# Optimization experiments

Hardware: AMD Instinct MI355X
Metric: run time of the kernel (lower is better)

The kernel has to match this reference:

```python
import jax, jax.numpy as jnp
import numpy as np

U = 100000
I = 100000
N = U + I          # total nodes
D = 64             # emb_size
E = 2000000        # nnz of normalized adjacency
B = 4096           # lookup batch
N_LAYERS = 3
ALPHA = 0.1
BETA = 0.9


def _spmm(rows, cols, vals, x):
    # y = A @ x for COO sparse A: y[r] += v * x[c]
    return jax.ops.segment_sum(vals[:, None] * x[cols], rows, num_segments=N)


def setup_inputs() -> dict:
    key = jax.random.key(0)
    ks = jax.random.split(key, 7)
    users = jax.random.randint(ks[0], (B,), 0, U, dtype=jnp.int32)
    items = jax.random.randint(ks[1], (B,), 0, I, dtype=jnp.int32)
    # xavier-uniform-ish init
    lim = float(np.sqrt(6.0 / (U + D)))
    user_emb = jax.random.uniform(ks[2], (U, D), jnp.float32, -lim, lim)
    item_emb = jax.random.uniform(ks[3], (I, D), jnp.float32, -lim, lim)
    adj_rows = jax.random.randint(ks[4], (E,), 0, N, dtype=jnp.int32)
    adj_cols = jax.random.randint(ks[5], (E,), 0, N, dtype=jnp.int32)
    # normalized adjacency values are small positives ~ 1/sqrt(deg_i*deg_j)
    adj_vals = jax.random.uniform(ks[6], (E,), jnp.float32, 0.0, 0.2)
    return {"users": users, "items": items, "user_emb": user_emb,
            "item_emb": item_emb, "adj_rows": adj_rows,
            "adj_cols": adj_cols, "adj_vals": adj_vals}


def reference(users, items, user_emb, item_emb, adj_rows, adj_cols, adj_vals):
    gamma = BETA ** N_LAYERS + ALPHA * sum(BETA ** i for i in range(N_LAYERS))
    ego = jnp.concatenate([user_emb, item_emb], axis=0)  # [N, D]
    x0 = jnp.zeros_like(ego)
    for k in range(N_LAYERS):
        ego = _spmm(adj_rows, adj_cols, adj_vals, ego)
        if k == 0:
            x0 = ego
        else:
            ego = ego * BETA + x0 * ALPHA
    ego = ego / gamma
    user_e = ego[:U][users]   # [B, D]
    item_e = ego[U:][items]   # [B, D]
    return (user_e, item_e)
```

## Files before the change

### kernel.cpp

```cpp
#include <hip/hip_runtime.h>
#include <hip/hip_fp16.h>

#define D 64
#define BETA 0.9f
#define ALPHA 0.1f
#define CB_SHIFT 10
#define CB_ROWS 1024
#define CAP_SHIFT 14
#define CAP (1 << CAP_SHIFT)

typedef __attribute__((ext_vector_type(16))) int int16v;

__global__ void concat_half(const float* __restrict__ u, const float* __restrict__ it,
                            long long UD, long long ND, __half* __restrict__ x) {
    long long n4 = ND >> 2;
    long long stride = (long long)gridDim.x * blockDim.x;
    for (long long i4 = (long long)blockIdx.x * blockDim.x + threadIdx.x; i4 < n4;
         i4 += stride) {
        long long base = i4 << 2;
        float4 v = (base < UD) ? ((const float4*)u)[i4]
                               : ((const float4*)it)[(base - UD) >> 2];
        __half2* dst = (__half2*)(x + base);
        dst[0] = __floats2half2_rn(v.x, v.y);
        dst[1] = __floats2half2_rn(v.z, v.w);
    }
}

__global__ void stageA(const int* __restrict__ rows, const int* __restrict__ cols,
                       const float* __restrict__ vals, int E,
                       int* __restrict__ gcur, int2* __restrict__ tmp) {
    __shared__ int hist[256];
    __shared__ int cur[256];
    int t = threadIdx.x;
    if (t < 256) hist[t] = 0;
    __syncthreads();
    int chunk = (E + gridDim.x - 1) / gridDim.x;
    int beg = blockIdx.x * chunk;
    int end = min(beg + chunk, E);
    for (int e = beg + t; e < end; e += blockDim.x)
        atomicAdd(&hist[rows[e] >> CB_SHIFT], 1);
    __syncthreads();
    if (t < 256) {
        int h = hist[t];
        cur[t] = h ? atomicAdd(&gcur[t], h) : 0;
    }
    __syncthreads();
    for (int e = beg + t; e < end; e += blockDim.x) {
        int r = rows[e];
        int cb = r >> CB_SHIFT;
        int p = atomicAdd(&cur[cb], 1);
        tmp[((size_t)cb << CAP_SHIFT) + p] =
            make_int2(cols[e] | ((r & (CB_ROWS - 1)) << 18), __float_as_int(vals[e]));
    }
}

__global__ void stageB(const int* __restrict__ bcnt, int N,
                       const int2* __restrict__ tmp,
                       int2* __restrict__ epack, int2* __restrict__ meta) {
    __shared__ int sc[CB_ROWS];
    __shared__ int cur[CB_ROWS];
    int cb = blockIdx.x;
    int t = threadIdx.x;
    size_t base = (size_t)cb << CAP_SHIFT;
    int nb = bcnt[cb];
    sc[t] = 0;
    __syncthreads();
    for (int e = t; e < nb; e += CB_ROWS)
        atomicAdd(&sc[((unsigned)tmp[base + e].x) >> 18], 1);
    __syncthreads();
    int mycnt = sc[t];
    for (int off = 1; off < CB_ROWS; off <<= 1) {
        int v = (t >= off) ? sc[t - off] : 0;
        __syncthreads();
        sc[t] += v;
        __syncthreads();
    }
    int excl = sc[t] - mycnt;
    cur[t] = excl;
    int r = (cb << CB_SHIFT) + t;
    if (r < N) meta[r] = make_int2((int)base + excl, mycnt);
    __syncthreads();
    for (int e = t; e < nb; e += CB_ROWS) {
        int2 pk = tmp[base + e];
        int rl = ((unsigned)pk.x) >> 18;
        int p = atomicAdd(&cur[rl], 1);
        epack[base + p] = make_int2(pk.x & ((1 << 18) - 1), pk.y);
    }
}

__device__ __forceinline__ float row_dot_s(const int2* __restrict__ ep,
                                           int beg, int cnt,
                                           const __half* __restrict__ x, int lane) {
    float acc = 0.f;
    int full = cnt & ~7;
    int e = 0;
    for (; e < full; e += 8) {
        int16v ed;
        asm volatile("s_load_dwordx16 %0, %1, 0x0\n\ts_waitcnt lgkmcnt(0)"
                     : "=s"(ed)
                     : "s"(ep + beg + e));
#define EDGEF(k)                                                              \
        acc += __int_as_float(ed[2 * (k) + 1]) *                              \
               __half2float(x[((size_t)ed[2 * (k)] << 6) + lane]);
        EDGEF(0) EDGEF(1) EDGEF(2) EDGEF(3) EDGEF(4) EDGEF(5) EDGEF(6) EDGEF(7)
#undef EDGEF
    }
    if (e < cnt) {
        int16v ed;
        asm volatile("s_load_dwordx16 %0, %1, 0x0\n\ts_waitcnt lgkmcnt(0)"
                     : "=s"(ed)
                     : "s"(ep + beg + e));
        int rem = cnt - e;
#define EDGET(k)                                                              \
        {                                                                     \
            int col = ((k) < rem) ? ed[2 * (k)] : 0;                          \
            float v = ((k) < rem) ? __int_as_float(ed[2 * (k) + 1]) : 0.0f;   \
            float xv = __half2float(x[((size_t)col << 6) + lane]);            \
            acc += ((k) < rem) ? v * xv : 0.0f;                               \
        }
        EDGET(0) EDGET(1) EDGET(2) EDGET(3) EDGET(4) EDGET(5) EDGET(6) EDGET(7)
#undef EDGET
    }
    return acc;
}

__global__ void spmm_l0(const int2* __restrict__ meta, const int2* __restrict__ epack,
                        const __half* __restrict__ xcat, int N, __half* __restrict__ y,
                        __half* __restrict__ ego1_row0) {
    int lane = threadIdx.x & 63;
    if (blockIdx.x == 0 && threadIdx.x < D)
        ego1_row0[threadIdx.x] = __float2half(0.0f);
    int r = blockIdx.x * (blockDim.x >> 6) + (threadIdx.x >> 6);
    if (r >= N) return;
    r = __builtin_amdgcn_readfirstlane(r);
    int2 m = meta[r];
    int beg = __builtin_amdgcn_readfirstlane(m.x);
    int cnt = __builtin_amdgcn_readfirstlane(m.y);
    float acc = row_dot_s(epack, beg, cnt, xcat, lane);
    y[((size_t)r << 6) + lane] = __float2half(acc);
}

__global__ void mark_flag2(const int* __restrict__ users, const int* __restrict__ items,
                           int B, int U, const int2* __restrict__ meta,
                           const int2* __restrict__ epack, int* __restrict__ flag2) {
    int lane = threadIdx.x & 63;
    int w = blockIdx.x * (blockDim.x >> 6) + (threadIdx.x >> 6);
    if (w >= 2 * B) return;
    int r = (w < B) ? users[w] : U + items[w - B];
    int2 m = meta[r];
    for (int e = m.x + lane; e < m.x + m.y; e += 64)
        flag2[epack[e].x] = 1;
}

__global__ void spmm_l1(const int2* __restrict__ meta, const int2* __restrict__ epack,
                        const __half* __restrict__ x0, const int* __restrict__ flag2,
                        int N, __half* __restrict__ y) {
    int lane = threadIdx.x & 63;
    int r = blockIdx.x * (blockDim.x >> 6) + (threadIdx.x >> 6);
    if (r >= N) return;
    r = __builtin_amdgcn_readfirstlane(r);
    if (flag2[r] == 0) return;
    int2 m = meta[r];
    int beg = __builtin_amdgcn_readfirstlane(m.x);
    int cnt = __builtin_amdgcn_readfirstlane(m.y);
    float acc = row_dot_s(epack, beg, cnt, x0, lane);
    float x0v = __half2float(x0[((size_t)r << 6) + lane]);
    y[((size_t)r << 6) + lane] = __float2half(BETA * acc + ALPHA * x0v);
}

__global__ void out_slots(const int* __restrict__ users, const int* __restrict__ items,
                          int B, int U,
                          const int2* __restrict__ meta, const int2* __restrict__ epack,
                          const __half* __restrict__ ego1, const __half* __restrict__ x0,
                          float inv_gamma, float* __restrict__ out) {
    int lane = threadIdx.x & 63;
    int w = blockIdx.x * (blockDim.x >> 6) + (threadIdx.x >> 6);
    if (w >= 2 * B) return;
    int r = (w < B) ? users[w] : U + items[w - B];
    r = __builtin_amdgcn_readfirstlane(r);
    int2 m = meta[r];
    int beg = __builtin_amdgcn_readfirstlane(m.x);
    int cnt = __builtin_amdgcn_readfirstlane(m.y);
    float acc = row_dot_s(epack, beg, cnt, ego1, lane);
    float x0v = __half2float(x0[((size_t)r << 6) + lane]);
    out[((size_t)w << 6) + lane] = (BETA * acc + ALPHA * x0v) * inv_gamma;
}

extern "C" void kernel_launch(void* const* d_in, const int* in_sizes, int n_in,
                              void* d_out, int out_size, void* d_ws, size_t ws_size,
                              hipStream_t stream) {
    const int*   users = (const int*)d_in[0];
    const int*   items = (const int*)d_in[1];
    const float* uemb  = (const float*)d_in[2];
    const float* iemb  = (const float*)d_in[3];
    const int*   arows = (const int*)d_in[4];
    const int*   acols = (const int*)d_in[5];
    const float* avals = (const float*)d_in[6];

    const int B = in_sizes[0];
    const int U = in_sizes[2] / D;
    const int I = in_sizes[3] / D;
    const int N = U + I;
    const int E = in_sizes[4];

    const double gamma_d = (double)BETA * BETA * BETA +
                           (double)ALPHA * (1.0 + (double)BETA + (double)BETA * BETA);
    const float inv_gamma = (float)(1.0 / gamma_d);

    const int NCB = (N + CB_ROWS - 1) / CB_ROWS;

    char* ws = (char*)d_ws;
    auto align256 = [](size_t x) { return (x + 255) & ~(size_t)255; };
    const size_t ndh_bytes = (size_t)N * D * sizeof(__half);
    const size_t cap_bytes = ((size_t)NCB << CAP_SHIFT) * sizeof(int2) + 64;
    __half* ego1   = (__half*)ws; ws += align256(ndh_bytes);
    int2*   tmp    = (int2*)ego1;
    __half* x0     = (__half*)ws; ws += align256(ndh_bytes);
    __half* xcat   = (__half*)ws; ws += align256(ndh_bytes);
    int2*  epack   = (int2*)ws;  ws += align256(cap_bytes);
    int2*  meta    = (int2*)ws;  ws += align256((size_t)N * sizeof(int2));
    int*   flag2   = (int*)ws;   ws += align256((size_t)N * sizeof(int));
    int*   gcur    = (int*)ws;   ws += align256(256 * sizeof(int));

    const int threads = 256;
    const int rows_per_block = threads / 64;

    concat_half<<<2048, threads, 0, stream>>>(uemb, iemb, (long long)U * D,
                                              (long long)N * D, xcat);

    hipMemsetAsync(gcur, 0, 256 * sizeof(int), stream);
    hipMemsetAsync(flag2, 0, (size_t)N * sizeof(int), stream);
    stageA<<<128, 1024, 0, stream>>>(arows, acols, avals, E, gcur, tmp);
    stageB<<<NCB, CB_ROWS, 0, stream>>>(gcur, N, tmp, epack, meta);

    const int spmm_grid = (N + rows_per_block - 1) / rows_per_block;
    const int slot_grid = (2 * B + rows_per_block - 1) / rows_per_block;

    spmm_l0<<<spmm_grid, threads, 0, stream>>>(meta, epack, xcat, N, x0, ego1);
    mark_flag2<<<slot_grid, threads, 0, stream>>>(users, items, B, U, meta, epack, flag2);
    spmm_l1<<<spmm_grid, threads, 0, stream>>>(meta, epack, x0, flag2, N, ego1);
    out_slots<<<slot_grid, threads, 0, stream>>>(users, items, B, U, meta, epack,
                                                 ego1, x0, inv_gamma, (float*)d_out);
}
```

Measured before the change: 173.1 us.

## Fuse prep kernels and flag marking into shared launches; widen edge batches to 16

Concat-to-half conversion, the flag2 clear and the stage-A bucketing now run in one launch split by block index, which removes a separate kernel and a memset. Flag marking is folded into the layer-0 SpMM launch as extra blocks. The row dot product issues two scalar 16-dword loads per iteration to handle 16 edges per batch, exposing more independent gathers. The cost is heavier tail handling for rows with few edges (up to 16 predicated gathers) and slightly more edge buffer padding.

```diff
diff --git a/kernel.cpp b/kernel.cpp
--- a/kernel.cpp
+++ b/kernel.cpp
@@ -8,49 +8,55 @@
 #define CB_ROWS 1024
 #define CAP_SHIFT 14
 #define CAP (1 << CAP_SHIFT)
+#define SA_BLOCKS 128
+#define CC_BLOCKS 256
 
 typedef __attribute__((ext_vector_type(16))) int int16v;
 
-__global__ void concat_half(const float* __restrict__ u, const float* __restrict__ it,
-                            long long UD, long long ND, __half* __restrict__ x) {
-    long long n4 = ND >> 2;
-    long long stride = (long long)gridDim.x * blockDim.x;
-    for (long long i4 = (long long)blockIdx.x * blockDim.x + threadIdx.x; i4 < n4;
-         i4 += stride) {
-        long long base = i4 << 2;
-        float4 v = (base < UD) ? ((const float4*)u)[i4]
-                               : ((const float4*)it)[(base - UD) >> 2];
-        __half2* dst = (__half2*)(x + base);
-        dst[0] = __floats2half2_rn(v.x, v.y);
-        dst[1] = __floats2half2_rn(v.z, v.w);
-    }
-}
-
-__global__ void stageA(const int* __restrict__ rows, const int* __restrict__ cols,
-                       const float* __restrict__ vals, int E,
-                       int* __restrict__ gcur, int2* __restrict__ tmp) {
+__global__ void prep(const int* __restrict__ rows, const int* __restrict__ cols,
+                     const float* __restrict__ vals, int E,
+                     int* __restrict__ gcur, int2* __restrict__ tmp,
+                     const float* __restrict__ u, const float* __restrict__ it,
+                     long long UD, long long ND, __half* __restrict__ x,
+                     int* __restrict__ flag2, int N) {
     __shared__ int hist[256];
     __shared__ int cur[256];
     int t = threadIdx.x;
-    if (t < 256) hist[t] = 0;
-    __syncthreads();
-    int chunk = (E + gridDim.x - 1) / gridDim.x;
-    int beg = blockIdx.x * chunk;
-    int end = min(beg + chunk, E);
-    for (int e = beg + t; e < end; e += blockDim.x)
-        atomicAdd(&hist[rows[e] >> CB_SHIFT], 1);
-    __syncthreads();
-    if (t < 256) {
-        int h = hist[t];
-        cur[t] = h ? atomicAdd(&gcur[t], h) : 0;
-    }
-    __syncthreads();
-    for (int e = beg + t; e < end; e += blockDim.x) {
-        int r = rows[e];
-        int cb = r >> CB_SHIFT;
-        int p = atomicAdd(&cur[cb], 1);
-        tmp[((size_t)cb << CAP_SHIFT) + p] =
-            make_int2(cols[e] | ((r & (CB_ROWS - 1)) << 18), __float_as_int(vals[e]));
+    if (blockIdx.x < SA_BLOCKS) {
+        if (t < 256) hist[t] = 0;
+        __syncthreads();
+        int chunk = (E + SA_BLOCKS - 1) / SA_BLOCKS;
+        int beg = blockIdx.x * chunk;
+        int end = min(beg + chunk, E);
+        for (int e = beg + t; e < end; e += 1024)
+            atomicAdd(&hist[rows[e] >> CB_SHIFT], 1);
+        __syncthreads();
+        if (t < 256) {
+            int h = hist[t];
+            cur[t] = h ? atomicAdd(&gcur[t], h) : 0;
+        }
+        __syncthreads();
+        for (int e = beg + t; e < end; e += 1024) {
+            int r = rows[e];
+            int cb = r >> CB_SHIFT;
+            int p = atomicAdd(&cur[cb], 1);
+            tmp[((size_t)cb << CAP_SHIFT) + p] =
+                make_int2(cols[e] | ((r & (CB_ROWS - 1)) << 18), __float_as_int(vals[e]));
+        }
+    } else {
+        int lb = blockIdx.x - SA_BLOCKS;
+        long long n4 = ND >> 2;
+        long long stride = (long long)CC_BLOCKS * 1024;
+        for (long long i4 = (long long)lb * 1024 + t; i4 < n4; i4 += stride) {
+            long long base = i4 << 2;
+            float4 v = (base < UD) ? ((const float4*)u)[i4]
+                                   : ((const float4*)it)[(base - UD) >> 2];
+            __half2* dst = (__half2*)(x + base);
+            dst[0] = __floats2half2_rn(v.x, v.y);
+            dst[1] = __floats2half2_rn(v.z, v.w);
+        }
+        for (long long i = (long long)lb * 1024 + t; i < N; i += stride)
+            flag2[i] = 0;
     }
 }
 
@@ -92,33 +98,44 @@
                                            int beg, int cnt,
                                            const __half* __restrict__ x, int lane) {
     float acc = 0.f;
-    int full = cnt & ~7;
     int e = 0;
-    for (; e < full; e += 8) {
-        int16v ed;
-        asm volatile("s_load_dwordx16 %0, %1, 0x0\n\ts_waitcnt lgkmcnt(0)"
-                     : "=s"(ed)
+    int full = cnt & ~15;
+    for (; e < full; e += 16) {
+        int16v ed0, ed1;
+        asm volatile("s_load_dwordx16 %0, %2, 0x0\n\t"
+                     "s_load_dwordx16 %1, %2, 0x40\n\t"
+                     "s_waitcnt lgkmcnt(0)"
+                     : "=s"(ed0), "=s"(ed1)
                      : "s"(ep + beg + e));
-#define EDGEF(k)                                                              \
-        acc += __int_as_float(ed[2 * (k) + 1]) *                              \
-               __half2float(x[((size_t)ed[2 * (k)] << 6) + lane]);
-        EDGEF(0) EDGEF(1) EDGEF(2) EDGEF(3) EDGEF(4) EDGEF(5) EDGEF(6) EDGEF(7)
+#define EDGEF(S, k)                                                           \
+        acc += __int_as_float(S[2 * (k) + 1]) *                               \
+               __half2float(x[((size_t)(unsigned)S[2 * (k)] << 6) + lane]);
+        EDGEF(ed0, 0) EDGEF(ed0, 1) EDGEF(ed0, 2) EDGEF(ed0, 3)
+        EDGEF(ed0, 4) EDGEF(ed0, 5) EDGEF(ed0, 6) EDGEF(ed0, 7)
+        EDGEF(ed1, 0) EDGEF(ed1, 1) EDGEF(ed1, 2) EDGEF(ed1, 3)
+        EDGEF(ed1, 4) EDGEF(ed1, 5) EDGEF(ed1, 6) EDGEF(ed1, 7)
 #undef EDGEF
     }
-    if (e < cnt) {
-        int16v ed;
-        asm volatile("s_load_dwordx16 %0, %1, 0x0\n\ts_waitcnt lgkmcnt(0)"
-                     : "=s"(ed)
+    int rem = cnt - e;
+    if (rem > 0) {
+        int16v ed0, ed1;
+        asm volatile("s_load_dwordx16 %0, %2, 0x0\n\t"
+                     "s_load_dwordx16 %1, %2, 0x40\n\t"
+                     "s_waitcnt lgkmcnt(0)"
+                     : "=s"(ed0), "=s"(ed1)
                      : "s"(ep + beg + e));
-        int rem = cnt - e;
-#define EDGET(k)                                                              \
+#define EDGET(S, k, b)                                                        \
         {                                                                     \
-            int col = ((k) < rem) ? ed[2 * (k)] : 0;                          \
-            float v = ((k) < rem) ? __int_as_float(ed[2 * (k) + 1]) : 0.0f;   \
-            float xv = __half2float(x[((size_t)col << 6) + lane]);            \
-            acc += ((k) < rem) ? v * xv : 0.0f;                               \
-        }
-        EDGET(0) EDGET(1) EDGET(2) EDGET(3) EDGET(4) EDGET(5) EDGET(6) EDGET(7)
+            bool ok = ((b) + (k)) < rem;                                      \
+            int col = ok ? S[2 * (k)] : 0;                                    \
+            float v = ok ? __int_as_float(S[2 * (k) + 1]) : 0.0f;             \
+            float xv = __half2float(x[((size_t)(unsigned)col << 6) + lane]);  \
+            acc += ok ? v * xv : 0.0f;                                        \
+        }
+        EDGET(ed0, 0, 0) EDGET(ed0, 1, 0) EDGET(ed0, 2, 0) EDGET(ed0, 3, 0)
+        EDGET(ed0, 4, 0) EDGET(ed0, 5, 0) EDGET(ed0, 6, 0) EDGET(ed0, 7, 0)
+        EDGET(ed1, 0, 8) EDGET(ed1, 1, 8) EDGET(ed1, 2, 8) EDGET(ed1, 3, 8)
+        EDGET(ed1, 4, 8) EDGET(ed1, 5, 8) EDGET(ed1, 6, 8) EDGET(ed1, 7, 8)
 #undef EDGET
     }
     return acc;
@@ -126,11 +143,23 @@
 
 __global__ void spmm_l0(const int2* __restrict__ meta, const int2* __restrict__ epack,
                         const __half* __restrict__ xcat, int N, __half* __restrict__ y,
-                        __half* __restrict__ ego1_row0) {
+                        __half* __restrict__ ego1_row0,
+                        const int* __restrict__ users, const int* __restrict__ items,
+                        int B, int U, int* __restrict__ flag2, int spmm_blocks) {
     int lane = threadIdx.x & 63;
+    int wv = threadIdx.x >> 6;
+    if (blockIdx.x >= spmm_blocks) {
+        int w = (blockIdx.x - spmm_blocks) * 4 + wv;
+        if (w >= 2 * B) return;
+        int r = (w < B) ? users[w] : U + items[w - B];
+        int2 m = meta[r];
+        for (int e = m.x + lane; e < m.x + m.y; e += 64)
+            flag2[epack[e].x] = 1;
+        return;
+    }
     if (blockIdx.x == 0 && threadIdx.x < D)
         ego1_row0[threadIdx.x] = __float2half(0.0f);
-    int r = blockIdx.x * (blockDim.x >> 6) + (threadIdx.x >> 6);
+    int r = blockIdx.x * 4 + wv;
     if (r >= N) return;
     r = __builtin_amdgcn_readfirstlane(r);
     int2 m = meta[r];
@@ -138,18 +167,6 @@
     int cnt = __builtin_amdgcn_readfirstlane(m.y);
     float acc = row_dot_s(epack, beg, cnt, xcat, lane);
     y[((size_t)r << 6) + lane] = __float2half(acc);
-}
-
-__global__ void mark_flag2(const int* __restrict__ users, const int* __restrict__ items,
-                           int B, int U, const int2* __restrict__ meta,
-                           const int2* __restrict__ epack, int* __restrict__ flag2) {
-    int lane = threadIdx.x & 63;
-    int w = blockIdx.x * (blockDim.x >> 6) + (threadIdx.x >> 6);
-    if (w >= 2 * B) return;
-    int r = (w < B) ? users[w] : U + items[w - B];
-    int2 m = meta[r];
-    for (int e = m.x + lane; e < m.x + m.y; e += 64)
-        flag2[epack[e].x] = 1;
 }
 
 __global__ void spmm_l1(const int2* __restrict__ meta, const int2* __restrict__ epack,
@@ -212,7 +229,7 @@
     char* ws = (char*)d_ws;
     auto align256 = [](size_t x) { return (x + 255) & ~(size_t)255; };
     const size_t ndh_bytes = (size_t)N * D * sizeof(__half);
-    const size_t cap_bytes = ((size_t)NCB << CAP_SHIFT) * sizeof(int2) + 64;
+    const size_t cap_bytes = ((size_t)NCB << CAP_SHIFT) * sizeof(int2) + 128;
     __half* ego1   = (__half*)ws; ws += align256(ndh_bytes);
     int2*   tmp    = (int2*)ego1;
     __half* x0     = (__half*)ws; ws += align256(ndh_bytes);
@@ -224,20 +241,18 @@
 
     const int threads = 256;
     const int rows_per_block = threads / 64;
-
-    concat_half<<<2048, threads, 0, stream>>>(uemb, iemb, (long long)U * D,
-                                              (long long)N * D, xcat);
-
-    hipMemsetAsync(gcur, 0, 256 * sizeof(int), stream);
-    hipMemsetAsync(flag2, 0, (size_t)N * sizeof(int), stream);
-    stageA<<<128, 1024, 0, stream>>>(arows, acols, avals, E, gcur, tmp);
-    stageB<<<NCB, CB_ROWS, 0, stream>>>(gcur, N, tmp, epack, meta);
-
     const int spmm_grid = (N + rows_per_block - 1) / rows_per_block;
     const int slot_grid = (2 * B + rows_per_block - 1) / rows_per_block;
 
-    spmm_l0<<<spmm_grid, threads, 0, stream>>>(meta, epack, xcat, N, x0, ego1);
-    mark_flag2<<<slot_grid, threads, 0, stream>>>(users, items, B, U, meta, epack, flag2);
+    hipMemsetAsync(gcur, 0, 256 * sizeof(int), stream);
+    prep<<<SA_BLOCKS + CC_BLOCKS, 1024, 0, stream>>>(arows, acols, avals, E, gcur, tmp,
+                                                     uemb, iemb, (long long)U * D,
+                                                     (long long)N * D, xcat, flag2, N);
+    stageB<<<NCB, CB_ROWS, 0, stream>>>(gcur, N, tmp, epack, meta);
+
+    spmm_l0<<<spmm_grid + slot_grid, threads, 0, stream>>>(meta, epack, xcat, N, x0, ego1,
+                                                           users, items, B, U, flag2,
+                                                           spmm_grid);
     spmm_l1<<<spmm_grid, threads, 0, stream>>>(meta, epack, x0, flag2, N, ego1);
     out_slots<<<slot_grid, threads, 0, stream>>>(users, items, B, U, meta, epack,
                                                  ego1, x0, inv_gamma, (float*)d_out);
```

Result: no change. 174.1 us (+0.6%).
